# Performance work log

Measured on AMD Instinct MI355X. Metric: run time of the kernel, lower is better.

The kernel has to match this reference:

```python
import jax, jax.numpy as jnp
import numpy as np

B, W, H = 8, 1024, 1024
NUM_LABELS = 100  # mask ids in [0, NUM_LABELS); 0 = background
EPS = 1e-7


def setup_inputs() -> dict:
    key = jax.random.key(0)
    k1, k2 = jax.random.split(key)
    pred = jax.random.normal(k1, (B, 2, W, H), dtype=jnp.float32)
    mask = jax.random.randint(k2, (B, W, H), 0, NUM_LABELS, dtype=jnp.int32)
    ignored_map = jnp.ones((B, W, H), dtype=jnp.float32)
    return {"pred": pred, "mask": mask, "ignored_map": ignored_map}


def _smooth_l1(d):
    # SmoothL1Loss(reduction='none'), beta=1
    a = jnp.abs(d)
    return jnp.where(a < 1.0, 0.5 * d * d, a - 0.5)


def _gt_single(mask2d):
    # Vectorized replacement of the per-instance python loop:
    # segment-mean for centroids, segment-max for the per-instance `norm`.
    seg = mask2d.reshape(-1)  # [W*H]
    x_map = jnp.tile(jnp.arange(H, dtype=jnp.float32), W)    # column index (x)
    y_map = jnp.repeat(jnp.arange(W, dtype=jnp.float32), H)  # row index (y)
    cnt = jax.ops.segment_sum(jnp.ones_like(x_map), seg, num_segments=NUM_LABELS)
    safe_cnt = jnp.maximum(cnt, 1.0)
    xc = (jax.ops.segment_sum(x_map, seg, num_segments=NUM_LABELS) / safe_cnt)[seg]
    yc = (jax.ops.segment_sum(y_map, seg, num_segments=NUM_LABELS) / safe_cnt)[seg]
    fg = (seg != 0).astype(jnp.float32)  # label 0 is background (index_list[1:])
    vx = (x_map - xc) * fg  # (x_map - mean_x) * nuclei, instances are disjoint
    vy = (y_map - yc) * fg
    # torch.max over the whole image of (coord - c)*nuclei == max(seg_max, 0)
    mx = jnp.maximum(jax.ops.segment_max(vx, seg, num_segments=NUM_LABELS), 0.0)
    my = jnp.maximum(jax.ops.segment_max(vy, seg, num_segments=NUM_LABELS), 0.0)
    gx = vx / jnp.where(mx == 0.0, 1.0, mx)[seg]  # norm(): divide by max iff max != 0
    gy = vy / jnp.where(my == 0.0, 1.0, my)[seg]
    return jnp.stack([gx, gy]).reshape(2, W, H)


def reference(pred, mask, ignored_map):
    gt = jax.vmap(_gt_single)(mask)  # [B, 2, W, H]
    fg = (mask != 0).astype(jnp.float32)[:, None]  # [B, 1, W, H]
    bg = 1.0 - fg
    n = float(mask.size)
    # ((mask != 0) + 1e-07).sum() == fg_count + eps * numel
    fg_den = jnp.sum(fg) + EPS * n
    bg_den = jnp.sum(bg) + EPS * n
    d = _smooth_l1(pred - gt)
    ig = ignored_map[:, None]
    offset_loss = jnp.sum(d * ig * (fg / fg_den + bg / bg_den))
    return offset_loss, gt
```

## Files before the change

### kernel.cpp

```cpp
#include <hip/hip_runtime.h>

#define NL 100
#define BB 8
#define HH 1024
#define NPIX (1024 * 1024)
#define EPSF 1e-7f
#define NBLK 128
#define LBLK 2048

typedef float f4 __attribute__((ext_vector_type(4)));

#define OFF_TAB  0
#define OFF_CNT0 3200
#define OFF_M8   3216
#define OFF_PART (OFF_M8 + BB * (NPIX / 4))
#define OFF_LP   (OFF_PART + 5 * NBLK * BB * NL)
#define WS_NEED  ((size_t)(OFF_LP + LBLK) * 4)

__device__ __forceinline__ int part_idx(int v, int blk, int b, int l) {
    return ((v * NBLK + blk) * BB + b) * NL + l;
}

template<bool EMIT8>
__global__ __launch_bounds__(256) void k_stats(const int* __restrict__ mask,
                                               unsigned* __restrict__ part,
                                               unsigned* __restrict__ m8) {
    __shared__ unsigned s_cs[4][2][NL];
    __shared__ unsigned s_mx[4][NL];
    __shared__ unsigned g_cnt[NL], g_sx[NL], g_sy[NL], g_mx[NL], g_my[NL];
    const int b    = blockIdx.y;
    const int wv   = threadIdx.x >> 6;
    const int lane = threadIdx.x & 63;
    for (int i = threadIdx.x; i < NL; i += 256) {
        g_cnt[i] = 0u; g_sx[i] = 0u; g_sy[i] = 0u; g_mx[i] = 0u; g_my[i] = 0u;
    }
    for (int i = lane; i < 2 * NL; i += 64) s_cs[wv][0][i] = 0u;
    for (int i = lane; i < NL; i += 64) s_mx[wv][i] = 0u;
    __syncthreads();

    const int4* m4  = (const int4*)(mask + (size_t)b * NPIX);
    unsigned*   m8b = m8 + (size_t)b * (NPIX / 4);
    const int y0 = blockIdx.x * 8 + wv * 2;

    int4 R[2][4];
#pragma unroll
    for (int r = 0; r < 2; ++r)
#pragma unroll
        for (int it = 0; it < 4; ++it)
            R[r][it] = m4[(y0 + r) * 256 + it * 64 + lane];

#pragma unroll
    for (int r = 0; r < 2; ++r) {
        unsigned* tp = &s_cs[wv][r][0];
        unsigned* mp = &s_mx[wv][0];
        const int y = y0 + r;
#pragma unroll
        for (int it = 0; it < 4; ++it) {
            const int4 mv = R[r][it];
            const int c4 = it * 64 + lane;
            const unsigned v0 = (1u << 21) + (unsigned)(c4 << 2);
            atomicAdd(tp + mv.x, v0);      atomicMax(mp + mv.x, v0);
            atomicAdd(tp + mv.y, v0 + 1u); atomicMax(mp + mv.y, v0 + 1u);
            atomicAdd(tp + mv.z, v0 + 2u); atomicMax(mp + mv.z, v0 + 2u);
            atomicAdd(tp + mv.w, v0 + 3u); atomicMax(mp + mv.w, v0 + 3u);
            if (EMIT8)
                m8b[y * 256 + c4] = (unsigned)mv.x | ((unsigned)mv.y << 8) |
                                    ((unsigned)mv.z << 16) | ((unsigned)mv.w << 24);
        }
    }
    for (int e = lane; e < NL; e += 64) {
        const unsigned cs0 = s_cs[wv][0][e];
        const unsigned cs1 = s_cs[wv][1][e];
        const unsigned c0 = cs0 >> 21, c1 = cs1 >> 21;
        const unsigned cnt = c0 + c1;
        if (cnt) {
            atomicAdd(&g_cnt[e], cnt);
            atomicAdd(&g_sx[e], (cs0 & 0x1FFFFFu) + (cs1 & 0x1FFFFFu));
            atomicAdd(&g_sy[e], c0 * (unsigned)y0 + c1 * (unsigned)(y0 + 1));
            atomicMax(&g_my[e], c1 ? (unsigned)(y0 + 1) : (unsigned)y0);
            atomicMax(&g_mx[e], s_mx[wv][e] & 0x1FFFFFu);
        }
    }
    __syncthreads();
    const int blk = blockIdx.x;
    for (int e = threadIdx.x; e < NL; e += 256) {
        part[part_idx(0, blk, b, e)] = g_cnt[e];
        part[part_idx(1, blk, b, e)] = g_sx[e];
        part[part_idx(2, blk, b, e)] = g_sy[e];
        part[part_idx(3, blk, b, e)] = g_mx[e];
        part[part_idx(4, blk, b, e)] = g_my[e];
    }
}

__global__ __launch_bounds__(512) void k_final(const unsigned* __restrict__ part,
                                               float* __restrict__ wsf) {
    __shared__ unsigned pc[4][NL], psx[4][NL], psy[4][NL], pmx[4][NL], pmy[4][NL];
    const int b = blockIdx.x;
    const int q = threadIdx.x >> 7;
    const int l = threadIdx.x & 127;
    if (l < NL) {
        unsigned cnt = 0, sx = 0, sy = 0, mx = 0, my = 0;
#pragma unroll 4
        for (int blk = q * 32; blk < q * 32 + 32; ++blk) {
            cnt += part[part_idx(0, blk, b, l)];
            sx  += part[part_idx(1, blk, b, l)];
            sy  += part[part_idx(2, blk, b, l)];
            mx = max(mx, part[part_idx(3, blk, b, l)]);
            my = max(my, part[part_idx(4, blk, b, l)]);
        }
        pc[q][l] = cnt; psx[q][l] = sx; psy[q][l] = sy; pmx[q][l] = mx; pmy[q][l] = my;
    }
    __syncthreads();
    if (q == 0 && l < NL) {
        const unsigned cnt = pc[0][l] + pc[1][l] + pc[2][l] + pc[3][l];
        const unsigned sx  = psx[0][l] + psx[1][l] + psx[2][l] + psx[3][l];
        const unsigned sy  = psy[0][l] + psy[1][l] + psy[2][l] + psy[3][l];
        const unsigned mx  = max(max(pmx[0][l], pmx[1][l]), max(pmx[2][l], pmx[3][l]));
        const unsigned my  = max(max(pmy[0][l], pmy[1][l]), max(pmy[2][l], pmy[3][l]));
        const float sc = (float)(cnt ? cnt : 1u);
        const float xc = (float)sx / sc;
        const float yc = (float)sy / sc;
        float fmx = (float)mx - xc; if (fmx < 0.0f) fmx = 0.0f;
        float fmy = (float)my - yc; if (fmy < 0.0f) fmy = 0.0f;
        f4 e;
        e.x = xc;
        e.y = yc;
        e.z = (fmx == 0.0f) ? 1.0f : 1.0f / fmx;
        e.w = (fmy == 0.0f) ? 1.0f : 1.0f / fmy;
        ((f4*)(wsf + OFF_TAB))[b * NL + l] = e;
        if (l == 0) ((unsigned*)wsf)[OFF_CNT0 + b] = cnt;
    }
}

template<bool USE8>
__global__ __launch_bounds__(256, 4) void k_loss(const int* __restrict__ mask,
                                                 const unsigned* __restrict__ m8,
                                                 const float* __restrict__ pred,
                                                 const float* __restrict__ ig,
                                                 const float* __restrict__ wsf,
                                                 float* __restrict__ lp,
                                                 float* __restrict__ out) {
    __shared__ f4 s_tab[NL];
    __shared__ unsigned s_c0[BB];
    const int b = blockIdx.y;
    for (int i = threadIdx.x; i < NL; i += 256)
        s_tab[i] = ((const f4*)(wsf + OFF_TAB))[b * NL + i];
    if (threadIdx.x < BB) s_c0[threadIdx.x] = ((const unsigned*)wsf)[OFF_CNT0 + threadIdx.x];
    __syncthreads();
    float bgc = 0.0f;
#pragma unroll
    for (int i = 0; i < BB; ++i) bgc += (float)s_c0[i];
    const float n = (float)BB * (float)NPIX;
    const float inv_bg = 1.0f / (bgc + EPSF * n);
    const float inv_fg = 1.0f / ((n - bgc) + EPSF * n);

    const int4*     mi4 = (const int4*)(mask + (size_t)b * NPIX);
    const unsigned* m8b = m8 + (size_t)b * (NPIX / 4);
    const f4*       ig4 = (const f4*)(ig + (size_t)b * NPIX);
    const f4*       px4 = (const f4*)(pred + (size_t)(2 * b) * NPIX);
    const f4*       py4 = (const f4*)(pred + (size_t)(2 * b + 1) * NPIX);
    f4* gx4 = (f4*)(out + 1 + (size_t)(2 * b) * NPIX);
    f4* gy4 = (f4*)(out + 1 + (size_t)(2 * b + 1) * NPIX);

    const int base = blockIdx.x * 1024;
    unsigned M8[4]; int4 MI[4]; f4 IV[4], PX[4], PY[4];
#pragma unroll
    for (int it = 0; it < 4; ++it) {
        const int i4 = base + it * 256 + threadIdx.x;
        if (USE8) M8[it] = m8b[i4]; else MI[it] = mi4[i4];
        IV[it] = __builtin_nontemporal_load(&ig4[i4]);
        PX[it] = __builtin_nontemporal_load(&px4[i4]);
        PY[it] = __builtin_nontemporal_load(&py4[i4]);
    }

    float acc = 0.0f;
#pragma unroll
    for (int it = 0; it < 4; ++it) {
        const int i4 = base + it * 256 + threadIdx.x;
        const int p  = i4 << 2;
        const float x0 = (float)(p & (HH - 1));
        const float y  = (float)(p >> 10);
        const float* igs = (const float*)&IV[it];
        const float* pxs = (const float*)&PX[it];
        const float* pys = (const float*)&PY[it];
        f4 gxv, gyv;
        float* gxa = (float*)&gxv;
        float* gya = (float*)&gyv;
#pragma unroll
        for (int j = 0; j < 4; ++j) {
            const int m = USE8 ? (int)((M8[it] >> (8 * j)) & 255u)
                               : ((const int*)&MI[it])[j];
            const f4 t = s_tab[m];
            const float fgf = (m != 0) ? 1.0f : 0.0f;
            const float gx = (x0 + (float)j - t.x) * t.z * fgf;
            const float gy = (y - t.y) * t.w * fgf;
            const float w  = ((m != 0) ? inv_fg : inv_bg) * igs[j];
            const float dx = pxs[j] - gx;
            const float dy = pys[j] - gy;
            const float ax = fabsf(dx), ay = fabsf(dy);
            acc += ((ax < 1.0f) ? 0.5f * dx * dx : ax - 0.5f) * w
                 + ((ay < 1.0f) ? 0.5f * dy * dy : ay - 0.5f) * w;
            gxa[j] = gx;
            gya[j] = gy;
        }
        __builtin_nontemporal_store(gxv, &gx4[i4]);
        __builtin_nontemporal_store(gyv, &gy4[i4]);
    }
#pragma unroll
    for (int off = 32; off > 0; off >>= 1) acc += __shfl_down(acc, off, 64);
    __shared__ float s_part[4];
    const int lane = threadIdx.x & 63, wv = threadIdx.x >> 6;
    if (lane == 0) s_part[wv] = acc;
    __syncthreads();
    if (threadIdx.x == 0) {
        const float s = s_part[0] + s_part[1] + s_part[2] + s_part[3];
        if (lp) lp[blockIdx.y * gridDim.x + blockIdx.x] = s;
        else    atomicAdd(out, s);
    }
}

__global__ __launch_bounds__(256) void k_sum(const float* __restrict__ lp,
                                             float* __restrict__ out) {
    float a = 0.0f;
#pragma unroll
    for (int i = threadIdx.x; i < LBLK; i += 256) a += lp[i];
#pragma unroll
    for (int off = 32; off > 0; off >>= 1) a += __shfl_down(a, off, 64);
    __shared__ float s[4];
    if ((threadIdx.x & 63) == 0) s[threadIdx.x >> 6] = a;
    __syncthreads();
    if (threadIdx.x == 0) out[0] = s[0] + s[1] + s[2] + s[3];
}

extern "C" void kernel_launch(void* const* d_in, const int* in_sizes, int n_in,
                              void* d_out, int out_size, void* d_ws, size_t ws_size,
                              hipStream_t stream) {
    const float* pred = (const float*)d_in[0];
    const int*   mask = (const int*)d_in[1];
    const float* ig   = (const float*)d_in[2];
    float* out = (float*)d_out;
    unsigned* wsu = (unsigned*)d_ws;

    const bool use8 = ws_size >= WS_NEED;
    unsigned* m8   = wsu + OFF_M8;
    unsigned* part = use8 ? (wsu + OFF_PART) : (wsu + OFF_M8);
    float*    lp   = use8 ? ((float*)wsu + OFF_LP) : nullptr;

    if (!use8) (void)hipMemsetAsync(d_out, 0, sizeof(float), stream);

    if (use8) k_stats<true ><<<dim3(NBLK, BB), 256, 0, stream>>>(mask, part, m8);
    else      k_stats<false><<<dim3(NBLK, BB), 256, 0, stream>>>(mask, part, m8);
    k_final<<<BB, 512, 0, stream>>>(part, (float*)d_ws);
    if (use8) k_loss<true ><<<dim3(256, BB), 256, 0, stream>>>(mask, m8, pred, ig, (const float*)d_ws, lp, out);
    else      k_loss<false><<<dim3(256, BB), 256, 0, stream>>>(mask, m8, pred, ig, (const float*)d_ws, lp, out);
    if (use8) k_sum<<<1, 256, 0, stream>>>(lp, out);
}
```

Baseline: 179.8 us.

## Fuse finalize and sum kernels into loss kernel with ticket-based reduction

Drops the separate finalize and final-sum kernels. Each loss block now reduces the per-block stats into its own per-image centroid/norm table, using a transposed partials layout so it can read them with vector loads. The final scalar is produced with a global atomic accumulator and a last-block ticket. The loss grid shrinks to 64 blocks per image, each covering four chunks, to amortize the redundant stats reduction. This removes two launches and their gaps, at the cost of recomputing the table in every block, lower occupancy, and a nondeterministic float atomic sum. The 8-bit mask path is now mandatory, with no fallback for a small workspace.

```diff
diff --git a/kernel.cpp b/kernel.cpp
--- a/kernel.cpp
+++ b/kernel.cpp
@@ -6,31 +6,36 @@
 #define NPIX (1024 * 1024)
 #define EPSF 1e-7f
 #define NBLK 128
-#define LBLK 2048
+#define LBK 64
+#define NLOSS (LBK * BB)
 
 typedef float f4 __attribute__((ext_vector_type(4)));
 
-#define OFF_TAB  0
-#define OFF_CNT0 3200
-#define OFF_M8   3216
+#define OFF_ACC  0
+#define OFF_TKT  1
+#define OFF_M8   8
 #define OFF_PART (OFF_M8 + BB * (NPIX / 4))
-#define OFF_LP   (OFF_PART + 5 * NBLK * BB * NL)
-#define WS_NEED  ((size_t)(OFF_LP + LBLK) * 4)
-
-__device__ __forceinline__ int part_idx(int v, int blk, int b, int l) {
-    return ((v * NBLK + blk) * BB + b) * NL + l;
-}
-
-template<bool EMIT8>
+#define WS_NEED  ((size_t)(OFF_PART + 5 * BB * NL * NBLK) * 4)
+
+__device__ __forceinline__ int pidx(int v, int b, int l) {
+    return ((v * BB + b) * NL + l) * NBLK;
+}
+
 __global__ __launch_bounds__(256) void k_stats(const int* __restrict__ mask,
-                                               unsigned* __restrict__ part,
-                                               unsigned* __restrict__ m8) {
+                                               unsigned* __restrict__ wsu) {
     __shared__ unsigned s_cs[4][2][NL];
     __shared__ unsigned s_mx[4][NL];
     __shared__ unsigned g_cnt[NL], g_sx[NL], g_sy[NL], g_mx[NL], g_my[NL];
+    unsigned* part = wsu + OFF_PART;
+    unsigned* m8   = wsu + OFF_M8;
     const int b    = blockIdx.y;
+    const int blk  = blockIdx.x;
     const int wv   = threadIdx.x >> 6;
     const int lane = threadIdx.x & 63;
+    if (blk == 0 && b == 0 && threadIdx.x == 0) {
+        ((float*)wsu)[OFF_ACC] = 0.0f;
+        wsu[OFF_TKT] = 0u;
+    }
     for (int i = threadIdx.x; i < NL; i += 256) {
         g_cnt[i] = 0u; g_sx[i] = 0u; g_sy[i] = 0u; g_mx[i] = 0u; g_my[i] = 0u;
     }
@@ -40,7 +45,7 @@
 
     const int4* m4  = (const int4*)(mask + (size_t)b * NPIX);
     unsigned*   m8b = m8 + (size_t)b * (NPIX / 4);
-    const int y0 = blockIdx.x * 8 + wv * 2;
+    const int y0 = blk * 8 + wv * 2;
 
     int4 R[2][4];
 #pragma unroll
@@ -63,9 +68,8 @@
             atomicAdd(tp + mv.y, v0 + 1u); atomicMax(mp + mv.y, v0 + 1u);
             atomicAdd(tp + mv.z, v0 + 2u); atomicMax(mp + mv.z, v0 + 2u);
             atomicAdd(tp + mv.w, v0 + 3u); atomicMax(mp + mv.w, v0 + 3u);
-            if (EMIT8)
-                m8b[y * 256 + c4] = (unsigned)mv.x | ((unsigned)mv.y << 8) |
-                                    ((unsigned)mv.z << 16) | ((unsigned)mv.w << 24);
+            m8b[y * 256 + c4] = (unsigned)mv.x | ((unsigned)mv.y << 8) |
+                                ((unsigned)mv.z << 16) | ((unsigned)mv.w << 24);
         }
     }
     for (int e = lane; e < NL; e += 64) {
@@ -82,70 +86,64 @@
         }
     }
     __syncthreads();
-    const int blk = blockIdx.x;
     for (int e = threadIdx.x; e < NL; e += 256) {
-        part[part_idx(0, blk, b, e)] = g_cnt[e];
-        part[part_idx(1, blk, b, e)] = g_sx[e];
-        part[part_idx(2, blk, b, e)] = g_sy[e];
-        part[part_idx(3, blk, b, e)] = g_mx[e];
-        part[part_idx(4, blk, b, e)] = g_my[e];
-    }
-}
-
-__global__ __launch_bounds__(512) void k_final(const unsigned* __restrict__ part,
-                                               float* __restrict__ wsf) {
-    __shared__ unsigned pc[4][NL], psx[4][NL], psy[4][NL], pmx[4][NL], pmy[4][NL];
-    const int b = blockIdx.x;
-    const int q = threadIdx.x >> 7;
-    const int l = threadIdx.x & 127;
-    if (l < NL) {
-        unsigned cnt = 0, sx = 0, sy = 0, mx = 0, my = 0;
-#pragma unroll 4
-        for (int blk = q * 32; blk < q * 32 + 32; ++blk) {
-            cnt += part[part_idx(0, blk, b, l)];
-            sx  += part[part_idx(1, blk, b, l)];
-            sy  += part[part_idx(2, blk, b, l)];
-            mx = max(mx, part[part_idx(3, blk, b, l)]);
-            my = max(my, part[part_idx(4, blk, b, l)]);
-        }
-        pc[q][l] = cnt; psx[q][l] = sx; psy[q][l] = sy; pmx[q][l] = mx; pmy[q][l] = my;
-    }
-    __syncthreads();
-    if (q == 0 && l < NL) {
-        const unsigned cnt = pc[0][l] + pc[1][l] + pc[2][l] + pc[3][l];
-        const unsigned sx  = psx[0][l] + psx[1][l] + psx[2][l] + psx[3][l];
-        const unsigned sy  = psy[0][l] + psy[1][l] + psy[2][l] + psy[3][l];
-        const unsigned mx  = max(max(pmx[0][l], pmx[1][l]), max(pmx[2][l], pmx[3][l]));
-        const unsigned my  = max(max(pmy[0][l], pmy[1][l]), max(pmy[2][l], pmy[3][l]));
+        part[pidx(0, b, e) + blk] = g_cnt[e];
+        part[pidx(1, b, e) + blk] = g_sx[e];
+        part[pidx(2, b, e) + blk] = g_sy[e];
+        part[pidx(3, b, e) + blk] = g_mx[e];
+        part[pidx(4, b, e) + blk] = g_my[e];
+    }
+}
+
+__global__ __launch_bounds__(256, 2) void k_loss(const float* __restrict__ pred,
+                                                 const float* __restrict__ ig,
+                                                 unsigned* __restrict__ wsu,
+                                                 float* __restrict__ out) {
+    __shared__ unsigned s_st[5][NL];
+    __shared__ unsigned s_c0[BB];
+    __shared__ f4 s_tab[NL];
+    __shared__ float s_red[4];
+    const unsigned* part = wsu + OFF_PART;
+    const unsigned* m8   = wsu + OFF_M8;
+    const int b   = blockIdx.y;
+    const int tid = threadIdx.x;
+
+    if (tid < BB) s_c0[tid] = 0u;
+    __syncthreads();
+    {
+        const int bb = tid >> 5, j = tid & 31;
+        const uint4* p4 = (const uint4*)(part + pidx(0, bb, 0));
+        const uint4 u = p4[j];
+        atomicAdd(&s_c0[bb], u.x + u.y + u.z + u.w);
+    }
+    for (int t = tid; t < 5 * NL; t += 256) {
+        const int v = t / NL;
+        const int l = t - v * NL;
+        const uint4* p4 = (const uint4*)(part + pidx(v, b, l));
+        unsigned s = 0u, m = 0u;
+#pragma unroll 8
+        for (int k = 0; k < NBLK / 4; ++k) {
+            const uint4 u = p4[k];
+            s += u.x + u.y + u.z + u.w;
+            m = max(max(m, u.x), max(u.y, max(u.z, u.w)));
+        }
+        s_st[v][l] = (v >= 3) ? m : s;
+    }
+    __syncthreads();
+    if (tid < NL) {
+        const unsigned cnt = s_st[0][tid];
         const float sc = (float)(cnt ? cnt : 1u);
-        const float xc = (float)sx / sc;
-        const float yc = (float)sy / sc;
-        float fmx = (float)mx - xc; if (fmx < 0.0f) fmx = 0.0f;
-        float fmy = (float)my - yc; if (fmy < 0.0f) fmy = 0.0f;
+        const float xc = (float)s_st[1][tid] / sc;
+        const float yc = (float)s_st[2][tid] / sc;
+        float fmx = (float)s_st[3][tid] - xc; if (fmx < 0.0f) fmx = 0.0f;
+        float fmy = (float)s_st[4][tid] - yc; if (fmy < 0.0f) fmy = 0.0f;
         f4 e;
         e.x = xc;
         e.y = yc;
         e.z = (fmx == 0.0f) ? 1.0f : 1.0f / fmx;
         e.w = (fmy == 0.0f) ? 1.0f : 1.0f / fmy;
-        ((f4*)(wsf + OFF_TAB))[b * NL + l] = e;
-        if (l == 0) ((unsigned*)wsf)[OFF_CNT0 + b] = cnt;
-    }
-}
-
-template<bool USE8>
-__global__ __launch_bounds__(256, 4) void k_loss(const int* __restrict__ mask,
-                                                 const unsigned* __restrict__ m8,
-                                                 const float* __restrict__ pred,
-                                                 const float* __restrict__ ig,
-                                                 const float* __restrict__ wsf,
-                                                 float* __restrict__ lp,
-                                                 float* __restrict__ out) {
-    __shared__ f4 s_tab[NL];
-    __shared__ unsigned s_c0[BB];
-    const int b = blockIdx.y;
-    for (int i = threadIdx.x; i < NL; i += 256)
-        s_tab[i] = ((const f4*)(wsf + OFF_TAB))[b * NL + i];
-    if (threadIdx.x < BB) s_c0[threadIdx.x] = ((const unsigned*)wsf)[OFF_CNT0 + threadIdx.x];
+        s_tab[tid] = e;
+    }
     __syncthreads();
     float bgc = 0.0f;
 #pragma unroll
@@ -154,82 +152,73 @@
     const float inv_bg = 1.0f / (bgc + EPSF * n);
     const float inv_fg = 1.0f / ((n - bgc) + EPSF * n);
 
-    const int4*     mi4 = (const int4*)(mask + (size_t)b * NPIX);
     const unsigned* m8b = m8 + (size_t)b * (NPIX / 4);
-    const f4*       ig4 = (const f4*)(ig + (size_t)b * NPIX);
-    const f4*       px4 = (const f4*)(pred + (size_t)(2 * b) * NPIX);
-    const f4*       py4 = (const f4*)(pred + (size_t)(2 * b + 1) * NPIX);
+    const f4* ig4 = (const f4*)(ig + (size_t)b * NPIX);
+    const f4* px4 = (const f4*)(pred + (size_t)(2 * b) * NPIX);
+    const f4* py4 = (const f4*)(pred + (size_t)(2 * b + 1) * NPIX);
     f4* gx4 = (f4*)(out + 1 + (size_t)(2 * b) * NPIX);
     f4* gy4 = (f4*)(out + 1 + (size_t)(2 * b + 1) * NPIX);
 
-    const int base = blockIdx.x * 1024;
-    unsigned M8[4]; int4 MI[4]; f4 IV[4], PX[4], PY[4];
-#pragma unroll
-    for (int it = 0; it < 4; ++it) {
-        const int i4 = base + it * 256 + threadIdx.x;
-        if (USE8) M8[it] = m8b[i4]; else MI[it] = mi4[i4];
-        IV[it] = __builtin_nontemporal_load(&ig4[i4]);
-        PX[it] = __builtin_nontemporal_load(&px4[i4]);
-        PY[it] = __builtin_nontemporal_load(&py4[i4]);
-    }
-
     float acc = 0.0f;
 #pragma unroll
-    for (int it = 0; it < 4; ++it) {
-        const int i4 = base + it * 256 + threadIdx.x;
-        const int p  = i4 << 2;
-        const float x0 = (float)(p & (HH - 1));
-        const float y  = (float)(p >> 10);
-        const float* igs = (const float*)&IV[it];
-        const float* pxs = (const float*)&PX[it];
-        const float* pys = (const float*)&PY[it];
-        f4 gxv, gyv;
-        float* gxa = (float*)&gxv;
-        float* gya = (float*)&gyv;
-#pragma unroll
-        for (int j = 0; j < 4; ++j) {
-            const int m = USE8 ? (int)((M8[it] >> (8 * j)) & 255u)
-                               : ((const int*)&MI[it])[j];
-            const f4 t = s_tab[m];
-            const float fgf = (m != 0) ? 1.0f : 0.0f;
-            const float gx = (x0 + (float)j - t.x) * t.z * fgf;
-            const float gy = (y - t.y) * t.w * fgf;
-            const float w  = ((m != 0) ? inv_fg : inv_bg) * igs[j];
-            const float dx = pxs[j] - gx;
-            const float dy = pys[j] - gy;
-            const float ax = fabsf(dx), ay = fabsf(dy);
-            acc += ((ax < 1.0f) ? 0.5f * dx * dx : ax - 0.5f) * w
-                 + ((ay < 1.0f) ? 0.5f * dy * dy : ay - 0.5f) * w;
-            gxa[j] = gx;
-            gya[j] = gy;
-        }
-        __builtin_nontemporal_store(gxv, &gx4[i4]);
-        __builtin_nontemporal_store(gyv, &gy4[i4]);
+    for (int g = 0; g < 4; ++g) {
+        const int base = (blockIdx.x * 4 + g) * 1024;
+        unsigned M8[4]; f4 IV[4], PX[4], PY[4];
+#pragma unroll
+        for (int it = 0; it < 4; ++it) {
+            const int i4 = base + it * 256 + tid;
+            M8[it] = m8b[i4];
+            IV[it] = __builtin_nontemporal_load(&ig4[i4]);
+            PX[it] = __builtin_nontemporal_load(&px4[i4]);
+            PY[it] = __builtin_nontemporal_load(&py4[i4]);
+        }
+#pragma unroll
+        for (int it = 0; it < 4; ++it) {
+            const int i4 = base + it * 256 + tid;
+            const int p  = i4 << 2;
+            const float x0 = (float)(p & (HH - 1));
+            const float y  = (float)(p >> 10);
+            const float* igs = (const float*)&IV[it];
+            const float* pxs = (const float*)&PX[it];
+            const float* pys = (const float*)&PY[it];
+            f4 gxv, gyv;
+            float* gxa = (float*)&gxv;
+            float* gya = (float*)&gyv;
+#pragma unroll
+            for (int j = 0; j < 4; ++j) {
+                const int m = (int)((M8[it] >> (8 * j)) & 255u);
+                const f4 t = s_tab[m];
+                const float fgf = (m != 0) ? 1.0f : 0.0f;
+                const float gx = (x0 + (float)j - t.x) * t.z * fgf;
+                const float gy = (y - t.y) * t.w * fgf;
+                const float w  = ((m != 0) ? inv_fg : inv_bg) * igs[j];
+                const float dx = pxs[j] - gx;
+                const float dy = pys[j] - gy;
+                const float ax = fabsf(dx), ay = fabsf(dy);
+                acc += ((ax < 1.0f) ? 0.5f * dx * dx : ax - 0.5f) * w
+                     + ((ay < 1.0f) ? 0.5f * dy * dy : ay - 0.5f) * w;
+                gxa[j] = gx;
+                gya[j] = gy;
+            }
+            __builtin_nontemporal_store(gxv, &gx4[i4]);
+            __builtin_nontemporal_store(gyv, &gy4[i4]);
+        }
     }
 #pragma unroll
     for (int off = 32; off > 0; off >>= 1) acc += __shfl_down(acc, off, 64);
-    __shared__ float s_part[4];
-    const int lane = threadIdx.x & 63, wv = threadIdx.x >> 6;
-    if (lane == 0) s_part[wv] = acc;
-    __syncthreads();
-    if (threadIdx.x == 0) {
-        const float s = s_part[0] + s_part[1] + s_part[2] + s_part[3];
-        if (lp) lp[blockIdx.y * gridDim.x + blockIdx.x] = s;
-        else    atomicAdd(out, s);
-    }
-}
-
-__global__ __launch_bounds__(256) void k_sum(const float* __restrict__ lp,
-                                             float* __restrict__ out) {
-    float a = 0.0f;
-#pragma unroll
-    for (int i = threadIdx.x; i < LBLK; i += 256) a += lp[i];
-#pragma unroll
-    for (int off = 32; off > 0; off >>= 1) a += __shfl_down(a, off, 64);
-    __shared__ float s[4];
-    if ((threadIdx.x & 63) == 0) s[threadIdx.x >> 6] = a;
-    __syncthreads();
-    if (threadIdx.x == 0) out[0] = s[0] + s[1] + s[2] + s[3];
+    const int lane = tid & 63, wv = tid >> 6;
+    if (lane == 0) s_red[wv] = acc;
+    __syncthreads();
+    if (tid == 0) {
+        const float s = s_red[0] + s_red[1] + s_red[2] + s_red[3];
+        atomicAdd((float*)wsu + OFF_ACC, s);
+        __threadfence();
+        const unsigned old = atomicAdd(wsu + OFF_TKT, 1u);
+        if (old == NLOSS - 1) {
+            __threadfence();
+            out[0] = atomicAdd((float*)wsu + OFF_ACC, 0.0f);
+        }
+    }
 }
 
 extern "C" void kernel_launch(void* const* d_in, const int* in_sizes, int n_in,
@@ -241,17 +230,6 @@
     float* out = (float*)d_out;
     unsigned* wsu = (unsigned*)d_ws;
 
-    const bool use8 = ws_size >= WS_NEED;
-    unsigned* m8   = wsu + OFF_M8;
-    unsigned* part = use8 ? (wsu + OFF_PART) : (wsu + OFF_M8);
-    float*    lp   = use8 ? ((float*)wsu + OFF_LP) : nullptr;
-
-    if (!use8) (void)hipMemsetAsync(d_out, 0, sizeof(float), stream);
-
-    if (use8) k_stats<true ><<<dim3(NBLK, BB), 256, 0, stream>>>(mask, part, m8);
-    else      k_stats<false><<<dim3(NBLK, BB), 256, 0, stream>>>(mask, part, m8);
-    k_final<<<BB, 512, 0, stream>>>(part, (float*)d_ws);
-    if (use8) k_loss<true ><<<dim3(256, BB), 256, 0, stream>>>(mask, m8, pred, ig, (const float*)d_ws, lp, out);
-    else      k_loss<false><<<dim3(256, BB), 256, 0, stream>>>(mask, m8, pred, ig, (const float*)d_ws, lp, out);
-    if (use8) k_sum<<<1, 256, 0, stream>>>(lp, out);
-}
+    k_stats<<<dim3(NBLK, BB), 256, 0, stream>>>(mask, wsu);
+    k_loss<<<dim3(LBK, BB), 256, 0, stream>>>(pred, ig, wsu, out);
+}
```

Measured after the change: 211.5 us. 17.6% more time.
